# Optimization experiments

Measured on AMD Instinct MI355X. Metric: run time of the kernel, lower is better.

The kernel has to match this reference:

```python
import jax, jax.numpy as jnp
import numpy as np

H = 128
OUT = 3
N_C = 50000
N_F = 150000
E_C = 400000
N_MP = 2


def _layernorm(x, g, b, eps=1e-5):
    mu = jnp.mean(x, axis=-1, keepdims=True)
    xc = x - mu
    var = jnp.mean(xc * xc, axis=-1, keepdims=True)
    return xc * jax.lax.rsqrt(var + eps) * g + b


def _seg_mean(v, idx, n):
    s = jax.ops.segment_sum(v, idx, num_segments=n)
    c = jax.ops.segment_sum(jnp.ones((v.shape[0],), v.dtype), idx, num_segments=n)
    return s / jnp.maximum(c, 1.0)[:, None]


def _mp_pass(x, ea, ei, n_nodes, eW0, eb0, eW1, eb1, eg, ebt, nW0, nb0, nW1, nb1, ng, nbt):
    src, dst = ei[0], ei[1]
    for i in range(N_MP):
        # edge update: gather endpoints, concat, 2-layer MLP, residual + LN
        t = jnp.concatenate([x[src], x[dst], ea], axis=1)  # [E, 3H]
        t = jax.nn.elu(t @ eW0[i] + eb0[i])
        t = t @ eW1[i] + eb1[i]
        ea = _layernorm(ea + t, eg[i], ebt[i])
        # scatter-mean aggregate edges to target nodes (EdgeAggregator)
        agg = _seg_mean(ea, dst, n_nodes)  # [N, H]
        xt = jnp.concatenate([x, agg], axis=1)  # [N, 2H]
        xt = jax.nn.elu(xt @ nW0[i] + nb0[i])
        xt = xt @ nW1[i] + nb1[i]
        x = _layernorm(x + xt, ng[i], nbt[i])
    return x, ea


def setup_inputs() -> dict:
    key = jax.random.key(0)
    ks = jax.random.split(key, 40)

    def nrm(k, shape, fan):
        return jax.random.normal(k, shape, jnp.float32) * np.float32(1.0 / np.sqrt(fan))

    inp = {}
    inp["x"] = jax.random.normal(ks[0], (N_C, H), jnp.float32)
    inp["edge_attr"] = jax.random.normal(ks[1], (E_C, H), jnp.float32)
    inp["pos_c"] = jax.random.uniform(ks[2], (N_C, 2), jnp.float32)
    inp["pos_f"] = jax.random.uniform(ks[3], (N_F, 2), jnp.float32)
    inp["edge_index_c"] = jax.random.randint(ks[4], (2, E_C), 0, N_C)
    clusters = jax.random.randint(ks[5], (N_F,), 0, N_C)
    inp["clusters"] = clusters
    # one f2c edge per fine node: row0 = fine idx, row1 = its coarse cluster
    inp["edge_index_f2c"] = jnp.stack([jnp.arange(N_F), clusters])
    # edge_up_mps params (stacked over N_MP layers)
    inp["eW0"] = nrm(ks[6], (N_MP, 3 * H, H), 3 * H)
    inp["eb0"] = jnp.zeros((N_MP, H), jnp.float32)
    inp["eW1"] = nrm(ks[7], (N_MP, H, H), H)
    inp["eb1"] = jnp.zeros((N_MP, H), jnp.float32)
    inp["eg"] = jnp.ones((N_MP, H), jnp.float32)
    inp["ebt"] = jnp.zeros((N_MP, H), jnp.float32)
    # node_up_mps params
    inp["nW0"] = nrm(ks[8], (N_MP, 2 * H, H), 2 * H)
    inp["nb0"] = jnp.zeros((N_MP, H), jnp.float32)
    inp["nW1"] = nrm(ks[9], (N_MP, H, H), H)
    inp["nb1"] = jnp.zeros((N_MP, H), jnp.float32)
    inp["ng"] = jnp.ones((N_MP, H), jnp.float32)
    inp["nbt"] = jnp.zeros((N_MP, H), jnp.float32)
    # edge_decoder_c2f_mlp
    inp["dW0"] = nrm(ks[10], (2, H), 2)
    inp["db0"] = jnp.zeros((H,), jnp.float32)
    inp["dW1"] = nrm(ks[11], (H, H), H)
    inp["db1"] = jnp.zeros((H,), jnp.float32)
    # upsample_mlp + norm
    inp["uW0"] = nrm(ks[12], (2 * H, H), 2 * H)
    inp["ub0"] = jnp.zeros((H,), jnp.float32)
    inp["uW1"] = nrm(ks[13], (H, H), H)
    inp["ub1"] = jnp.zeros((H,), jnp.float32)
    inp["ug"] = jnp.ones((H,), jnp.float32)
    inp["ubt"] = jnp.zeros((H,), jnp.float32)
    # output embedding
    inp["oW"] = nrm(ks[14], (H, OUT), H)
    inp["ob"] = jnp.zeros((OUT,), jnp.float32)
    return inp


def reference(x, edge_attr, pos_c, pos_f, edge_index_c, clusters, edge_index_f2c,
              eW0, eb0, eW1, eb1, eg, ebt, nW0, nb0, nW1, nb1, ng, nbt,
              dW0, db0, dW1, db1, uW0, ub0, uW1, ub1, ug, ubt, oW, ob):
    # coarse-level message passing (m = 0)
    x, ea = _mp_pass(x, edge_attr, edge_index_c, N_C,
                     eW0, eb0, eW1, eb1, eg, ebt, nW0, nb0, nW1, nb1, ng, nbt)
    # upsample coarse -> fine (depth = 2, l_char[0] = 1.0)
    c2f = edge_index_f2c[::-1]  # row0 = coarse idx, row1 = fine idx
    eac = (pos_c[c2f[0]] - pos_f[c2f[1]]) / 1.0  # [N_F, 2]
    eac = jax.nn.elu(eac @ dW0 + db0)
    eac = jax.nn.elu(eac @ dW1 + db1)
    xg = x[clusters]  # [N_F, H]
    t = jnp.concatenate([eac, xg], axis=1)
    t = jax.nn.elu(t @ uW0 + ub0)
    t = jax.nn.elu(t @ uW1 + ub1)
    t = _layernorm(eac + t, ug, ubt)
    x = _seg_mean(t, c2f[1], N_F)  # aggregate c2f edges onto fine nodes
    # fine-level message passing (m stays 0 in the original code -> same weights, same coarse edges)
    x, ea = _mp_pass(x, ea, edge_index_c, N_F,
                     eW0, eb0, eW1, eb1, eg, ebt, nW0, nb0, nW1, nb1, ng, nbt)
    x = jax.nn.elu(x @ oW + ob)
    return (x, edge_index_c)
```

## Files before the change

### kernel.cpp

```cpp
#include <hip/hip_runtime.h>


#define HD   128
#define NC   50000
#define NF   150000
#define ECNT 400000
#define OUTD 3
#define SCB  512
#define NB_SCAN ((NF + SCB - 1) / SCB)

typedef unsigned short u16;
typedef unsigned int   u32;
typedef short bf16x8 __attribute__((ext_vector_type(8)));
typedef float f32x4  __attribute__((ext_vector_type(4)));

__device__ __forceinline__ float bf2f(u32 u){ return __uint_as_float(u << 16); }
__device__ __forceinline__ u32 cvtpk(float a, float b){
  u32 r; asm("v_cvt_pk_bf16_f32 %0, %1, %2" : "=v"(r) : "v"(a), "v"(b)); return r;
}
__device__ __forceinline__ u16 f2bf(float f){ return (u16)cvtpk(f, f); }
__device__ __forceinline__ u32 addpk(u32 a, u32 b){
  return cvtpk(bf2f(a & 0xffffu) + bf2f(b & 0xffffu),
               __uint_as_float(a & 0xffff0000u) + __uint_as_float(b & 0xffff0000u));
}
__device__ __forceinline__ float eluf(float x){ return x > 0.f ? x : __expf(x) - 1.f; }
__device__ __forceinline__ int SW(int row, int byte){ return row * 256 + (byte ^ ((row & 7) << 4)); }


__global__ void prep_all_kernel(const float* __restrict__ eW0, const float* __restrict__ eW1,
                                const float* __restrict__ nW0, const float* __restrict__ nW1,
                                const float* __restrict__ uW0, const float* __restrict__ uW1,
                                const float* __restrict__ dW1,
                                u16* c_eW0, u16* c_eW1, u16* c_nW0, u16* c_nW1,
                                u16* c_uW0, u16* c_uW1, u16* c_dW1)
{
  int b = blockIdx.x;
  const float* src; u16* dst; int kb;
  if      (b <  384){ src = eW0; dst = c_eW0; kb = b * 2; }
  else if (b <  512){ src = eW1; dst = c_eW1; kb = (b - 384) * 2; }
  else if (b <  768){ src = nW0; dst = c_nW0; kb = (b - 512) * 2; }
  else if (b <  896){ src = nW1; dst = c_nW1; kb = (b - 768) * 2; }
  else if (b < 1024){ src = uW0; dst = c_uW0; kb = (b - 896) * 2; }
  else if (b < 1088){ src = uW1; dst = c_uW1; kb = (b - 1024) * 2; }
  else              { src = dW1; dst = c_dW1; kb = (b - 1088) * 2; }
  int t = threadIdx.x;
  int k = kb + (t >> 7), j = t & 127;
  dst[(((k >> 3) * HD + j) << 3) + (k & 7)] = f2bf(src[k * HD + j]);
}

__global__ void f32_to_bf16_vec(const float* __restrict__ in, u16* __restrict__ out, int n8){
  int i = blockIdx.x * blockDim.x + threadIdx.x;
  if (i >= n8) return;
  float4 f0 = ((const float4*)in)[i * 2];
  float4 f1 = ((const float4*)in)[i * 2 + 1];
  ((uint4*)out)[i] = make_uint4(cvtpk(f0.x,f0.y), cvtpk(f0.z,f0.w), cvtpk(f1.x,f1.y), cvtpk(f1.z,f1.w));
}

__global__ void deg_kernel(const int* __restrict__ ei, int* __restrict__ deg){
  int e = blockIdx.x * blockDim.x + threadIdx.x;
  if (e < ECNT) atomicAdd(&deg[ei[ECNT + e]], 1);
}

__global__ void scanA_kernel(const int* __restrict__ deg, int* __restrict__ part){
  __shared__ int s[SCB];
  int t = threadIdx.x, i = blockIdx.x * SCB + t;
  s[t] = (i < NF) ? deg[i] : 0;
  __syncthreads();
  for (int off = SCB/2; off; off >>= 1){ if (t < off) s[t] += s[t + off]; __syncthreads(); }
  if (t == 0) part[blockIdx.x] = s[0];
}

__global__ void scanB_kernel(int* __restrict__ part){
  __shared__ int s[SCB];
  int t = threadIdx.x;
  int v = (t < NB_SCAN) ? part[t] : 0;
  s[t] = v; __syncthreads();
  for (int off = 1; off < SCB; off <<= 1){
    int x = (t >= off) ? s[t - off] : 0;
    __syncthreads(); s[t] += x; __syncthreads();
  }
  if (t < NB_SCAN) part[t] = s[t] - v;
}

__global__ void scanC_kernel(const int* __restrict__ deg, const int* __restrict__ part,
                             int* __restrict__ rowptr){
  __shared__ int s[SCB];
  int t = threadIdx.x, i = blockIdx.x * SCB + t;
  int v = (i < NF) ? deg[i] : 0;
  s[t] = v; __syncthreads();
  for (int off = 1; off < SCB; off <<= 1){
    int x = (t >= off) ? s[t - off] : 0;
    __syncthreads(); s[t] += x; __syncthreads();
  }
  int excl = part[blockIdx.x] + s[t] - v;
  if (i < NF) rowptr[i] = excl;
  if (i == NF - 1) rowptr[NF] = excl + v;
}

__global__ void build_perm_kernel(const int* __restrict__ ei, int* __restrict__ cursor,
                                  int* __restrict__ perm, int* __restrict__ esrc,
                                  int* __restrict__ edst){
  int e = blockIdx.x * blockDim.x + threadIdx.x;
  if (e >= ECNT) return;
  int sI = ei[e], d = ei[ECNT + e];
  int p = atomicAdd(&cursor[d], 1);
  perm[p] = e; esrc[p] = sI; edst[p] = d;
}

__global__ void permute_ea_kernel(const float* __restrict__ ea_in, const int* __restrict__ perm,
                                  u16* __restrict__ ea_s){
  int i = blockIdx.x * blockDim.x + threadIdx.x;
  if (i >= ECNT * 16) return;
  int p = i >> 4, c = i & 15;
  int e = perm[p];
  const float4* src = (const float4*)(ea_in + (size_t)e * HD + c * 8);
  float4 f0 = src[0], f1 = src[1];
  ((uint4*)ea_s)[(size_t)p * 16 + c] =
      make_uint4(cvtpk(f0.x,f0.y), cvtpk(f0.z,f0.w), cvtpk(f1.x,f1.y), cvtpk(f1.z,f1.w));
}

template<int NOUT>
__global__ __launch_bounds__(256, 4)
void lin_kernel(const u16* __restrict__ Wa, const u16* __restrict__ Wb, const u16* __restrict__ Wc,
                const u16* __restrict__ x, u16* __restrict__ oA, u16* __restrict__ oB,
                u16* __restrict__ oC, int nA, int nB, int nC, int n_rows)
{
  __shared__ __align__(16) char ldsA[32 * 256];
  const int tid = threadIdx.x, lane = tid & 63, wid = tid >> 6;
  const int ln = lane & 15, kq = lane >> 4, ncol = wid * 32;

  const int row0 = blockIdx.x << 5;
  #pragma unroll
  for (int c = 0; c < 2; ++c){
    int i = tid + c * 256, row = i >> 4, kk = i & 15, rg = row0 + row;
    if (rg < n_rows)
      *(uint4*)(ldsA + SW(row, kk * 16)) = *(const uint4*)(x + (((size_t)rg) << 7) + (kk << 3));
  }
  __syncthreads();
  bf16x8 af[4][2];
  #pragma unroll
  for (int k0 = 0; k0 < 4; ++k0){
    af[k0][0] = *(const bf16x8*)(ldsA + SW(ln,      k0 * 64 + (kq << 4)));
    af[k0][1] = *(const bf16x8*)(ldsA + SW(16 + ln, k0 * 64 + (kq << 4)));
  }

  const u16* Ws[3] = {Wa, Wb, Wc};
  u16*       Os[3] = {oA, oB, oC};
  const int  Ns[3] = {nA, nB, nC};
  const f32x4 zz = {0.f, 0.f, 0.f, 0.f};
  #pragma unroll
  for (int w = 0; w < NOUT; ++w){
    if (row0 < Ns[w]){
      const u16* wp = Ws[w];
      asm volatile("" : "+v"(wp));
      uint4 bfr[4][2];
      #pragma unroll
      for (int k0 = 0; k0 < 4; ++k0)
        #pragma unroll
        for (int nt = 0; nt < 2; ++nt)
          bfr[k0][nt] = *(const uint4*)(wp + (((size_t)((k0*4 + kq)*HD + ncol + nt*16 + ln)) << 3));
      f32x4 cc[2][2] = {{zz, zz}, {zz, zz}};
      #pragma unroll
      for (int k0 = 0; k0 < 4; ++k0){
        bf16x8 w0 = __builtin_bit_cast(bf16x8, bfr[k0][0]);
        bf16x8 w1 = __builtin_bit_cast(bf16x8, bfr[k0][1]);
        cc[0][0] = __builtin_amdgcn_mfma_f32_16x16x32_bf16(af[k0][0], w0, cc[0][0], 0, 0, 0);
        cc[0][1] = __builtin_amdgcn_mfma_f32_16x16x32_bf16(af[k0][0], w1, cc[0][1], 0, 0, 0);
        cc[1][0] = __builtin_amdgcn_mfma_f32_16x16x32_bf16(af[k0][1], w0, cc[1][0], 0, 0, 0);
        cc[1][1] = __builtin_amdgcn_mfma_f32_16x16x32_bf16(af[k0][1], w1, cc[1][1], 0, 0, 0);
      }
      u16* op = Os[w];
      #pragma unroll
      for (int mi = 0; mi < 2; ++mi)
        #pragma unroll
        for (int nt = 0; nt < 2; ++nt)
          #pragma unroll
          for (int r = 0; r < 4; ++r){
            int rg = row0 + mi * 16 + kq * 4 + r;
            if (rg < Ns[w]) op[(size_t)rg * HD + ncol + nt * 16 + ln] = f2bf(cc[mi][nt][r]);
          }
    }
  }
}

enum { M_EDGE = 0, M_NODE = 1, M_DEC12 = 2 };

template<int MODE>
__global__ __launch_bounds__(256, 4)
void mlp_kernel(const u16* __restrict__ W0c, const u16* __restrict__ W1c,
                const u16* __restrict__ W2c,
                const float* __restrict__ b0, const float* __restrict__ b1,
                const float* __restrict__ b2,
                const float* __restrict__ gw, const float* __restrict__ bw,
                const u16* __restrict__ tabA, const u16* __restrict__ addP,
                const u16* __restrict__ addQ, const u16* __restrict__ resid,
                const int* __restrict__ esrc, const int* __restrict__ edst,
                const int* __restrict__ rowptr, const u16* __restrict__ eatab,
                const int* __restrict__ clus,
                u16* __restrict__ outp, int n_rows,
                const float* __restrict__ dW0, const float* __restrict__ db0,
                const float* __restrict__ pos_c, const float* __restrict__ pos_f)
{
  constexpr bool RESLDS = (MODE == M_EDGE || MODE == M_DEC12);

  __shared__ __align__(16) char ldsA [32 * 256];
  __shared__ __align__(16) char ldsPQ[32 * 256];

  const int tid  = threadIdx.x;
  const int lane = tid & 63;
  const int wid  = tid >> 6;
  const int ln   = lane & 15, kq = lane >> 4;
  const int ncol = wid * 32;

  bf16x8 b1f[4][2];
  #pragma unroll
  for (int k0 = 0; k0 < 4; ++k0)
    #pragma unroll
    for (int nt = 0; nt < 2; ++nt)
      b1f[k0][nt] = *(const bf16x8*)(W0c + (((size_t)((k0*4 + kq)*HD + ncol + nt*16 + ln)) << 3));

  float b0v[2], b1v[2], b2v[2] = {0.f, 0.f};
  #pragma unroll
  for (int nt = 0; nt < 2; ++nt){ b0v[nt] = b0[ncol + nt*16 + ln]; b1v[nt] = b1[ncol + nt*16 + ln]; }
  if constexpr (MODE == M_DEC12){
    #pragma unroll
    for (int nt = 0; nt < 2; ++nt) b2v[nt] = b2[ncol + nt*16 + ln];
  }
  float gl0 = gw[lane], gl1 = gw[64 + lane], bt0 = bw[lane], bt1 = bw[64 + lane];

  const int row0 = blockIdx.x << 5;

  if constexpr (MODE == M_EDGE){
    #pragma unroll
    for (int c = 0; c < 2; ++c){
      int i = tid + c * 256, row = i >> 4, kk = i & 15, rg = row0 + row;
      *(uint4*)(ldsA + SW(row, kk * 16)) =
          *(const uint4*)(tabA + (((size_t)rg) << 7) + (kk << 3));
      int sI = esrc[rg], dI = edst[rg];
      uint4 p = *(const uint4*)(addP + (((size_t)sI) << 7) + (kk << 3));
      uint4 q = *(const uint4*)(addQ + (((size_t)dI) << 7) + (kk << 3));
      *(uint4*)(ldsPQ + SW(row, kk * 16)) =
          make_uint4(addpk(p.x,q.x), addpk(p.y,q.y), addpk(p.z,q.z), addpk(p.w,q.w));
    }
  } else if constexpr (MODE == M_NODE){
    #pragma unroll
    for (int c = 0; c < 2; ++c){
      int i = tid + c * 256, row = i >> 4, kk = i & 15, rg = row0 + row;
      if (rg < n_rows)
        *(uint4*)(ldsPQ + SW(row, kk * 16)) =
            *(const uint4*)(addP + (((size_t)rg) << 7) + (kk << 3));
    }
    for (int s = 0; s < 8; ++s){
      int nd = wid * 8 + s, rg = row0 + nd;
      if (rg < n_rows){
        int rp0 = rowptr[rg], rp1 = rowptr[rg + 1];
        float s0 = 0.f, s1 = 0.f, t0 = 0.f, t1 = 0.f;
        int i2 = rp0;
        for (; i2 + 3 < rp1; i2 += 4){
          u32 ua = *(const u32*)(eatab + (((size_t) i2     ) << 7) + (lane << 1));
          u32 ub = *(const u32*)(eatab + (((size_t)(i2 + 1)) << 7) + (lane << 1));
          u32 uc = *(const u32*)(eatab + (((size_t)(i2 + 2)) << 7) + (lane << 1));
          u32 ud = *(const u32*)(eatab + (((size_t)(i2 + 3)) << 7) + (lane << 1));
          s0 += bf2f(ua & 0xffffu) + bf2f(ub & 0xffffu);
          s1 += bf2f(ua >> 16)     + bf2f(ub >> 16);
          t0 += bf2f(uc & 0xffffu) + bf2f(ud & 0xffffu);
          t1 += bf2f(uc >> 16)     + bf2f(ud >> 16);
        }
        for (; i2 < rp1; ++i2){
          u32 ua = *(const u32*)(eatab + (((size_t)i2) << 7) + (lane << 1));
          s0 += bf2f(ua & 0xffffu); s1 += bf2f(ua >> 16);
        }
        s0 += t0; s1 += t1;
        int dg = rp1 - rp0;
        float rd = 1.f / (float)(dg > 0 ? dg : 1);
        *(u32*)(ldsA + SW(nd, lane << 2)) = cvtpk(s0 * rd, s1 * rd);
      }
    }
  } else {
    #pragma unroll
    for (int c = 0; c < 2; ++c){
      int i = tid + c * 256, row = i >> 4, c8 = i & 15, rg = row0 + row;
      if (rg < n_rows){
        int cl = clus[rg];
        *(uint4*)(ldsPQ + SW(row, c8 * 16)) =
            *(const uint4*)(addP + (((size_t)cl) << 7) + (c8 << 3));
        float d0 = pos_c[cl * 2]     - pos_f[rg * 2];
        float d1 = pos_c[cl * 2 + 1] - pos_f[rg * 2 + 1];
        u32 wq[4];
        #pragma unroll
        for (int q = 0; q < 4; ++q){
          int cc = c8 * 8 + q * 2;
          float va = eluf(fmaf(d0, dW0[cc],     fmaf(d1, dW0[HD + cc],     db0[cc])));
          float vb = eluf(fmaf(d0, dW0[cc + 1], fmaf(d1, dW0[HD + cc + 1], db0[cc + 1])));
          wq[q] = cvtpk(va, vb);
        }
        *(uint4*)(ldsA + SW(row, c8 * 16)) = make_uint4(wq[0], wq[1], wq[2], wq[3]);
      }
    }
  }
  __syncthreads();

  const f32x4 zz = {0.f, 0.f, 0.f, 0.f};
  f32x4 c1[2][2] = {{zz, zz}, {zz, zz}};
  #pragma unroll
  for (int k0 = 0; k0 < 4; ++k0){
    bf16x8 a0 = *(const bf16x8*)(ldsA + SW(ln,      k0 * 64 + (kq << 4)));
    bf16x8 a1 = *(const bf16x8*)(ldsA + SW(16 + ln, k0 * 64 + (kq << 4)));
    c1[0][0] = __builtin_amdgcn_mfma_f32_16x16x32_bf16(a0, b1f[k0][0], c1[0][0], 0, 0, 0);
    c1[0][1] = __builtin_amdgcn_mfma_f32_16x16x32_bf16(a0, b1f[k0][1], c1[0][1], 0, 0, 0);
    c1[1][0] = __builtin_amdgcn_mfma_f32_16x16x32_bf16(a1, b1f[k0][0], c1[1][0], 0, 0, 0);
    c1[1][1] = __builtin_amdgcn_mfma_f32_16x16x32_bf16(a1, b1f[k0][1], c1[1][1], 0, 0, 0);
  }

  if constexpr (MODE == M_DEC12){
    __syncthreads();
    #pragma unroll
    for (int mi = 0; mi < 2; ++mi)
      #pragma unroll
      for (int nt = 0; nt < 2; ++nt)
        #pragma unroll
        for (int r = 0; r < 4; ++r){
          int row = mi * 16 + kq * 4 + r, col = ncol + nt * 16 + ln;
          *(u16*)(ldsA + SW(row, col * 2)) = f2bf(eluf(c1[mi][nt][r] + b0v[nt]));
        }
    __syncthreads();

    {
      const u16* w1p = W1c;
      asm volatile("" : "+v"(w1p));
      uint4 b2r[4][2];
      #pragma unroll
      for (int k0 = 0; k0 < 4; ++k0)
        #pragma unroll
        for (int nt = 0; nt < 2; ++nt)
          b2r[k0][nt] = *(const uint4*)(w1p + (((size_t)((k0*4 + kq)*HD + ncol + nt*16 + ln)) << 3));
      f32x4 c2[2][2] = {{zz, zz}, {zz, zz}};
      #pragma unroll
      for (int k0 = 0; k0 < 4; ++k0){
        bf16x8 a0 = *(const bf16x8*)(ldsA + SW(ln,      k0 * 64 + (kq << 4)));
        bf16x8 a1 = *(const bf16x8*)(ldsA + SW(16 + ln, k0 * 64 + (kq << 4)));
        bf16x8 w0 = __builtin_bit_cast(bf16x8, b2r[k0][0]);
        bf16x8 w1 = __builtin_bit_cast(bf16x8, b2r[k0][1]);
        c2[0][0] = __builtin_amdgcn_mfma_f32_16x16x32_bf16(a0, w0, c2[0][0], 0, 0, 0);
        c2[0][1] = __builtin_amdgcn_mfma_f32_16x16x32_bf16(a0, w1, c2[0][1], 0, 0, 0);
        c2[1][0] = __builtin_amdgcn_mfma_f32_16x16x32_bf16(a1, w0, c2[1][0], 0, 0, 0);
        c2[1][1] = __builtin_amdgcn_mfma_f32_16x16x32_bf16(a1, w1, c2[1][1], 0, 0, 0);
      }
      #pragma unroll
      for (int mi = 0; mi < 2; ++mi)
        #pragma unroll
        for (int nt = 0; nt < 2; ++nt)
          #pragma unroll
          for (int r = 0; r < 4; ++r){
            int row = mi * 16 + kq * 4 + r, col = ncol + nt * 16 + ln;
            u16* pp = (u16*)(ldsPQ + SW(row, col * 2));
            float pq = bf2f(*pp);
            *pp = f2bf(eluf(c2[mi][nt][r] + pq + b1v[nt]));
          }
    }
    __syncthreads();

    {
      const u16* w2p = W2c;
      asm volatile("" : "+v"(w2p));
      uint4 b3r[4][2];
      #pragma unroll
      for (int k0 = 0; k0 < 4; ++k0)
        #pragma unroll
        for (int nt = 0; nt < 2; ++nt)
          b3r[k0][nt] = *(const uint4*)(w2p + (((size_t)((k0*4 + kq)*HD + ncol + nt*16 + ln)) << 3));
      f32x4 c3[2][2] = {{zz, zz}, {zz, zz}};
      #pragma unroll
      for (int k0 = 0; k0 < 4; ++k0){
        bf16x8 a0 = *(const bf16x8*)(ldsPQ + SW(ln,      k0 * 64 + (kq << 4)));
        bf16x8 a1 = *(const bf16x8*)(ldsPQ + SW(16 + ln, k0 * 64 + (kq << 4)));
        bf16x8 w0 = __builtin_bit_cast(bf16x8, b3r[k0][0]);
        bf16x8 w1 = __builtin_bit_cast(bf16x8, b3r[k0][1]);
        c3[0][0] = __builtin_amdgcn_mfma_f32_16x16x32_bf16(a0, w0, c3[0][0], 0, 0, 0);
        c3[0][1] = __builtin_amdgcn_mfma_f32_16x16x32_bf16(a0, w1, c3[0][1], 0, 0, 0);
        c3[1][0] = __builtin_amdgcn_mfma_f32_16x16x32_bf16(a1, w0, c3[1][0], 0, 0, 0);
        c3[1][1] = __builtin_amdgcn_mfma_f32_16x16x32_bf16(a1, w1, c3[1][1], 0, 0, 0);
      }
      __syncthreads();
      #pragma unroll
      for (int mi = 0; mi < 2; ++mi)
        #pragma unroll
        for (int nt = 0; nt < 2; ++nt)
          #pragma unroll
          for (int r = 0; r < 4; ++r){
            int row = mi * 16 + kq * 4 + r, col = ncol + nt * 16 + ln;
            *(u16*)(ldsPQ + SW(row, col * 2)) = f2bf(eluf(c3[mi][nt][r] + b2v[nt]));
          }
    }
    __syncthreads();
  } else {
    const u16* w1p = W1c;
    asm volatile("" : "+v"(w1p));
    uint4 b2r[4][2];
    #pragma unroll
    for (int k0 = 0; k0 < 4; ++k0)
      #pragma unroll
      for (int nt = 0; nt < 2; ++nt)
        b2r[k0][nt] = *(const uint4*)(w1p + (((size_t)((k0*4 + kq)*HD + ncol + nt*16 + ln)) << 3));

    #pragma unroll
    for (int mi = 0; mi < 2; ++mi)
      #pragma unroll
      for (int nt = 0; nt < 2; ++nt)
        #pragma unroll
        for (int r = 0; r < 4; ++r){
          int row = mi * 16 + kq * 4 + r, col = ncol + nt * 16 + ln;
          u16* pp = (u16*)(ldsPQ + SW(row, col * 2));
          float pq = bf2f(*pp);
          *pp = f2bf(eluf(c1[mi][nt][r] + pq + b0v[nt]));
        }
    __syncthreads();

    f32x4 c2[2][2] = {{zz, zz}, {zz, zz}};
    #pragma unroll
    for (int k0 = 0; k0 < 4; ++k0){
      bf16x8 a0 = *(const bf16x8*)(ldsPQ + SW(ln,      k0 * 64 + (kq << 4)));
      bf16x8 a1 = *(const bf16x8*)(ldsPQ + SW(16 + ln, k0 * 64 + (kq << 4)));
      bf16x8 w0 = __builtin_bit_cast(bf16x8, b2r[k0][0]);
      bf16x8 w1 = __builtin_bit_cast(bf16x8, b2r[k0][1]);
      c2[0][0] = __builtin_amdgcn_mfma_f32_16x16x32_bf16(a0, w0, c2[0][0], 0, 0, 0);
      c2[0][1] = __builtin_amdgcn_mfma_f32_16x16x32_bf16(a0, w1, c2[0][1], 0, 0, 0);
      c2[1][0] = __builtin_amdgcn_mfma_f32_16x16x32_bf16(a1, w0, c2[1][0], 0, 0, 0);
      c2[1][1] = __builtin_amdgcn_mfma_f32_16x16x32_bf16(a1, w1, c2[1][1], 0, 0, 0);
    }
    __syncthreads();

    #pragma unroll
    for (int mi = 0; mi < 2; ++mi)
      #pragma unroll
      for (int nt = 0; nt < 2; ++nt)
        #pragma unroll
        for (int r = 0; r < 4; ++r){
          int row = mi * 16 + kq * 4 + r, col = ncol + nt * 16 + ln;
          *(u16*)(ldsPQ + SW(row, col * 2)) = f2bf(c2[mi][nt][r] + b1v[nt]);
        }
    __syncthreads();
  }

  #pragma unroll
  for (int rr = 0; rr < 8; ++rr){
    int e = wid * 8 + rr, rg = row0 + e;
    float v0 = bf2f(*(const u16*)(ldsPQ + SW(e, lane * 2)));
    float v1 = bf2f(*(const u16*)(ldsPQ + SW(e, (64 + lane) * 2)));
    if constexpr (RESLDS){
      v0 += bf2f(*(const u16*)(ldsA + SW(e, lane * 2)));
      v1 += bf2f(*(const u16*)(ldsA + SW(e, (64 + lane) * 2)));
    } else if (rg < n_rows){
      v0 += bf2f(resid[(((size_t)rg) << 7) + lane]);
      v1 += bf2f(resid[(((size_t)rg) << 7) + 64 + lane]);
    }
    float s = v0 + v1, q = v0 * v0 + v1 * v1;
    #pragma unroll
    for (int o = 32; o; o >>= 1){ s += __shfl_xor(s, o); q += __shfl_xor(q, o); }
    float mu  = s * (1.f / 128.f);
    float var = q * (1.f / 128.f) - mu * mu;
    float rs  = rsqrtf(var + 1e-5f);
    float y0 = (v0 - mu) * rs * gl0 + bt0;
    float y1 = (v1 - mu) * rs * gl1 + bt1;
    if (rg < n_rows){
      outp[(((size_t)rg) << 7) + lane]      = f2bf(y0);
      outp[(((size_t)rg) << 7) + 64 + lane] = f2bf(y1);
    }
  }
}

__global__ void outhead_kernel(const u16* __restrict__ x, const float* __restrict__ oW,
                               const float* __restrict__ ob, float* __restrict__ out){
  int row  = (blockIdx.x * blockDim.x + threadIdx.x) >> 6;
  int lane = threadIdx.x & 63;
  if (row >= NF) return;
  float x0 = bf2f(x[((size_t)row << 7) + lane]);
  float x1 = bf2f(x[((size_t)row << 7) + 64 + lane]);
  float s0 = x0 * oW[lane * 3 + 0] + x1 * oW[(64 + lane) * 3 + 0];
  float s1 = x0 * oW[lane * 3 + 1] + x1 * oW[(64 + lane) * 3 + 1];
  float s2 = x0 * oW[lane * 3 + 2] + x1 * oW[(64 + lane) * 3 + 2];
  #pragma unroll
  for (int o = 32; o; o >>= 1){
    s0 += __shfl_xor(s0, o); s1 += __shfl_xor(s1, o); s2 += __shfl_xor(s2, o);
  }
  if (lane == 0){
    out[row * 3 + 0] = eluf(s0 + ob[0]);
    out[row * 3 + 1] = eluf(s1 + ob[1]);
    out[row * 3 + 2] = eluf(s2 + ob[2]);
  }
}

__global__ void idxcopy_kernel(const int* __restrict__ ei, float* __restrict__ out){
  int i = blockIdx.x * blockDim.x + threadIdx.x;
  if (i < 2 * ECNT) out[i] = (float)ei[i];
}

extern "C" void kernel_launch(void* const* d_in, const int* in_sizes, int n_in,
                              void* d_out, int out_size, void* d_ws, size_t ws_size,
                              hipStream_t stream)
{
  const float* x_in  = (const float*)d_in[0];
  const float* ea_in = (const float*)d_in[1];
  const float* pos_c = (const float*)d_in[2];
  const float* pos_f = (const float*)d_in[3];
  const int*   ei    = (const int*)d_in[4];
  const int*   clus  = (const int*)d_in[5];
  const float* eW0 = (const float*)d_in[7];
  const float* eb0 = (const float*)d_in[8];
  const float* eW1 = (const float*)d_in[9];
  const float* eb1 = (const float*)d_in[10];
  const float* eg  = (const float*)d_in[11];
  const float* ebt = (const float*)d_in[12];
  const float* nW0 = (const float*)d_in[13];
  const float* nb0 = (const float*)d_in[14];
  const float* nW1 = (const float*)d_in[15];
  const float* nb1 = (const float*)d_in[16];
  const float* ng  = (const float*)d_in[17];
  const float* nbt = (const float*)d_in[18];
  const float* dW0 = (const float*)d_in[19];
  const float* db0 = (const float*)d_in[20];
  const float* dW1 = (const float*)d_in[21];
  const float* db1 = (const float*)d_in[22];
  const float* uW0 = (const float*)d_in[23];
  const float* ub0 = (const float*)d_in[24];
  const float* uW1 = (const float*)d_in[25];
  const float* ub1 = (const float*)d_in[26];
  const float* ug  = (const float*)d_in[27];
  const float* ubt = (const float*)d_in[28];
  const float* oW  = (const float*)d_in[29];
  const float* ob  = (const float*)d_in[30];

  char* w = (char*)d_ws;
  auto alloc = [&](size_t bytes) -> char* {
    char* p = w; w += (bytes + 255) & ~(size_t)255; return p;
  };
  u16*   ea_s   = (u16*)alloc((size_t)ECNT * HD * 2);
  u16*   xa     = (u16*)alloc((size_t)NC * HD * 2);
  u16*   xb     = (u16*)alloc((size_t)NF * HD * 2);
  u16*   P      = (u16*)alloc((size_t)NF * HD * 2);
  u16*   Q      = (u16*)alloc((size_t)NF * HD * 2);
  u16*   T      = (u16*)alloc((size_t)NF * HD * 2);
  u16*   XU     = (u16*)alloc((size_t)NC * HD * 2);
  int*   deg    = (int*)alloc((size_t)NF * 4);
  int*   rowptr = (int*)alloc((size_t)(NF + 1) * 4);
  int*   cursor = (int*)alloc((size_t)NF * 4);
  int*   perm   = (int*)alloc((size_t)ECNT * 4);
  int*   esrc   = (int*)alloc((size_t)ECNT * 4);
  int*   edst   = (int*)alloc((size_t)ECNT * 4);
  int*   part   = (int*)alloc((size_t)SCB * 4);
  u16*   c_eW0  = (u16*)alloc((size_t)2 * 384 * HD * 2);
  u16*   c_eW1  = (u16*)alloc((size_t)2 * HD * HD * 2);
  u16*   c_nW0  = (u16*)alloc((size_t)2 * 256 * HD * 2);
  u16*   c_nW1  = (u16*)alloc((size_t)2 * HD * HD * 2);
  u16*   c_uW0  = (u16*)alloc((size_t)256 * HD * 2);
  u16*   c_uW1  = (u16*)alloc((size_t)HD * HD * 2);
  u16*   c_dW1  = (u16*)alloc((size_t)HD * HD * 2);

  prep_all_kernel<<<1152, 256, 0, stream>>>(eW0, eW1, nW0, nW1, uW0, uW1, dW1,
                                            c_eW0, c_eW1, c_nW0, c_nW1, c_uW0, c_uW1, c_dW1);
  f32_to_bf16_vec<<<(NC * HD / 8 + 255) / 256, 256, 0, stream>>>(x_in, xa, NC * HD / 8);

  hipMemsetAsync(deg, 0, (size_t)NF * 4, stream);
  deg_kernel<<<(ECNT + 255) / 256, 256, 0, stream>>>(ei, deg);
  scanA_kernel<<<NB_SCAN, SCB, 0, stream>>>(deg, part);
  scanB_kernel<<<1, SCB, 0, stream>>>(part);
  scanC_kernel<<<NB_SCAN, SCB, 0, stream>>>(deg, part, rowptr);
  hipMemcpyAsync(cursor, rowptr, (size_t)NF * 4, hipMemcpyDeviceToDevice, stream);
  build_perm_kernel<<<(ECNT + 255) / 256, 256, 0, stream>>>(ei, cursor, perm, esrc, edst);
  permute_ea_kernel<<<(ECNT * 16 + 255) / 256, 256, 0, stream>>>(ea_in, perm, ea_s);

  auto grd = [](int rows){ return (rows + 31) / 32; };
  const int KS = 16 * HD * 8;

  auto mp_iter = [&](u16* x, int n, int i){
    int npq = n < NC ? n : NC;
    lin_kernel<3><<<grd(n), 256, 0, stream>>>(
      c_eW0 + (size_t)i*384*HD, c_eW0 + (size_t)i*384*HD + KS, c_nW0 + (size_t)i*256*HD,
      x, P, Q, T, npq, npq, n, n);
    mlp_kernel<M_EDGE><<<grd(ECNT), 256, 0, stream>>>(
      c_eW0 + (size_t)i*384*HD + 2*KS, c_eW1 + (size_t)i*HD*HD, nullptr,
      eb0 + i*HD, eb1 + i*HD, nullptr, eg + i*HD, ebt + i*HD,
      ea_s, P, Q, nullptr, esrc, edst, nullptr, nullptr, nullptr,
      ea_s, ECNT, nullptr, nullptr, nullptr, nullptr);
    mlp_kernel<M_NODE><<<grd(n), 256, 0, stream>>>(
      c_nW0 + (size_t)i*256*HD + KS, c_nW1 + (size_t)i*HD*HD, nullptr,
      nb0 + i*HD, nb1 + i*HD, nullptr, ng + i*HD, nbt + i*HD,
      nullptr, T, nullptr, x, nullptr, nullptr, rowptr, ea_s, nullptr,
      x, n, nullptr, nullptr, nullptr, nullptr);
  };

  mp_iter(xa, NC, 0);
  mp_iter(xa, NC, 1);

  lin_kernel<1><<<grd(NC), 256, 0, stream>>>(
    c_uW0 + KS, nullptr, nullptr, xa, XU, nullptr, nullptr, NC, 0, 0, NC);
  mlp_kernel<M_DEC12><<<grd(NF), 256, 0, stream>>>(
    c_dW1, c_uW0, c_uW1,
    db1, ub0, ub1, ug, ubt,
    nullptr, XU, nullptr, nullptr,
    nullptr, nullptr, nullptr, nullptr, clus,
    xb, NF, dW0, db0, pos_c, pos_f);

  mp_iter(xb, NF, 0);
  mp_iter(xb, NF, 1);

  float* out = (float*)d_out;
  outhead_kernel<<<(NF + 3) / 4, 256, 0, stream>>>(xb, oW, ob, out);
  idxcopy_kernel<<<(2 * ECNT + 255) / 256, 256, 0, stream>>>(ei, out + (size_t)NF * OUTD);
}
```

Before: 983.0 us.

## Fuse node-side x@W0 projection into node MLP kernel and skip aggregation for edgeless rows

```diff
diff --git a/kernel.cpp b/kernel.cpp
--- a/kernel.cpp
+++ b/kernel.cpp
@@ -121,9 +121,9 @@
 
 template<int NOUT>
 __global__ __launch_bounds__(256, 4)
-void lin_kernel(const u16* __restrict__ Wa, const u16* __restrict__ Wb, const u16* __restrict__ Wc,
+void lin_kernel(const u16* __restrict__ Wa, const u16* __restrict__ Wb,
                 const u16* __restrict__ x, u16* __restrict__ oA, u16* __restrict__ oB,
-                u16* __restrict__ oC, int nA, int nB, int nC, int n_rows)
+                int n_rows)
 {
   __shared__ __align__(16) char ldsA[32 * 256];
   const int tid = threadIdx.x, lane = tid & 63, wid = tid >> 6;
@@ -144,42 +144,39 @@
     af[k0][1] = *(const bf16x8*)(ldsA + SW(16 + ln, k0 * 64 + (kq << 4)));
   }
 
-  const u16* Ws[3] = {Wa, Wb, Wc};
-  u16*       Os[3] = {oA, oB, oC};
-  const int  Ns[3] = {nA, nB, nC};
+  const u16* Ws[2] = {Wa, Wb};
+  u16*       Os[2] = {oA, oB};
   const f32x4 zz = {0.f, 0.f, 0.f, 0.f};
   #pragma unroll
   for (int w = 0; w < NOUT; ++w){
-    if (row0 < Ns[w]){
-      const u16* wp = Ws[w];
-      asm volatile("" : "+v"(wp));
-      uint4 bfr[4][2];
-      #pragma unroll
-      for (int k0 = 0; k0 < 4; ++k0)
-        #pragma unroll
-        for (int nt = 0; nt < 2; ++nt)
-          bfr[k0][nt] = *(const uint4*)(wp + (((size_t)((k0*4 + kq)*HD + ncol + nt*16 + ln)) << 3));
-      f32x4 cc[2][2] = {{zz, zz}, {zz, zz}};
-      #pragma unroll
-      for (int k0 = 0; k0 < 4; ++k0){
-        bf16x8 w0 = __builtin_bit_cast(bf16x8, bfr[k0][0]);
-        bf16x8 w1 = __builtin_bit_cast(bf16x8, bfr[k0][1]);
-        cc[0][0] = __builtin_amdgcn_mfma_f32_16x16x32_bf16(af[k0][0], w0, cc[0][0], 0, 0, 0);
-        cc[0][1] = __builtin_amdgcn_mfma_f32_16x16x32_bf16(af[k0][0], w1, cc[0][1], 0, 0, 0);
-        cc[1][0] = __builtin_amdgcn_mfma_f32_16x16x32_bf16(af[k0][1], w0, cc[1][0], 0, 0, 0);
-        cc[1][1] = __builtin_amdgcn_mfma_f32_16x16x32_bf16(af[k0][1], w1, cc[1][1], 0, 0, 0);
-      }
-      u16* op = Os[w];
-      #pragma unroll
-      for (int mi = 0; mi < 2; ++mi)
-        #pragma unroll
-        for (int nt = 0; nt < 2; ++nt)
-          #pragma unroll
-          for (int r = 0; r < 4; ++r){
-            int rg = row0 + mi * 16 + kq * 4 + r;
-            if (rg < Ns[w]) op[(size_t)rg * HD + ncol + nt * 16 + ln] = f2bf(cc[mi][nt][r]);
-          }
-    }
+    const u16* wp = Ws[w];
+    asm volatile("" : "+v"(wp));
+    uint4 bfr[4][2];
+    #pragma unroll
+    for (int k0 = 0; k0 < 4; ++k0)
+      #pragma unroll
+      for (int nt = 0; nt < 2; ++nt)
+        bfr[k0][nt] = *(const uint4*)(wp + (((size_t)((k0*4 + kq)*HD + ncol + nt*16 + ln)) << 3));
+    f32x4 cc[2][2] = {{zz, zz}, {zz, zz}};
+    #pragma unroll
+    for (int k0 = 0; k0 < 4; ++k0){
+      bf16x8 w0 = __builtin_bit_cast(bf16x8, bfr[k0][0]);
+      bf16x8 w1 = __builtin_bit_cast(bf16x8, bfr[k0][1]);
+      cc[0][0] = __builtin_amdgcn_mfma_f32_16x16x32_bf16(af[k0][0], w0, cc[0][0], 0, 0, 0);
+      cc[0][1] = __builtin_amdgcn_mfma_f32_16x16x32_bf16(af[k0][0], w1, cc[0][1], 0, 0, 0);
+      cc[1][0] = __builtin_amdgcn_mfma_f32_16x16x32_bf16(af[k0][1], w0, cc[1][0], 0, 0, 0);
+      cc[1][1] = __builtin_amdgcn_mfma_f32_16x16x32_bf16(af[k0][1], w1, cc[1][1], 0, 0, 0);
+    }
+    u16* op = Os[w];
+    #pragma unroll
+    for (int mi = 0; mi < 2; ++mi)
+      #pragma unroll
+      for (int nt = 0; nt < 2; ++nt)
+        #pragma unroll
+        for (int r = 0; r < 4; ++r){
+          int rg = row0 + mi * 16 + kq * 4 + r;
+          if (rg < n_rows) op[(size_t)rg * HD + ncol + nt * 16 + ln] = f2bf(cc[mi][nt][r]);
+        }
   }
 }
 
@@ -247,34 +244,8 @@
     for (int c = 0; c < 2; ++c){
       int i = tid + c * 256, row = i >> 4, kk = i & 15, rg = row0 + row;
       if (rg < n_rows)
-        *(uint4*)(ldsPQ + SW(row, kk * 16)) =
-            *(const uint4*)(addP + (((size_t)rg) << 7) + (kk << 3));
-    }
-    for (int s = 0; s < 8; ++s){
-      int nd = wid * 8 + s, rg = row0 + nd;
-      if (rg < n_rows){
-        int rp0 = rowptr[rg], rp1 = rowptr[rg + 1];
-        float s0 = 0.f, s1 = 0.f, t0 = 0.f, t1 = 0.f;
-        int i2 = rp0;
-        for (; i2 + 3 < rp1; i2 += 4){
-          u32 ua = *(const u32*)(eatab + (((size_t) i2     ) << 7) + (lane << 1));
-          u32 ub = *(const u32*)(eatab + (((size_t)(i2 + 1)) << 7) + (lane << 1));
-          u32 uc = *(const u32*)(eatab + (((size_t)(i2 + 2)) << 7) + (lane << 1));
-          u32 ud = *(const u32*)(eatab + (((size_t)(i2 + 3)) << 7) + (lane << 1));
-          s0 += bf2f(ua & 0xffffu) + bf2f(ub & 0xffffu);
-          s1 += bf2f(ua >> 16)     + bf2f(ub >> 16);
-          t0 += bf2f(uc & 0xffffu) + bf2f(ud & 0xffffu);
-          t1 += bf2f(uc >> 16)     + bf2f(ud >> 16);
-        }
-        for (; i2 < rp1; ++i2){
-          u32 ua = *(const u32*)(eatab + (((size_t)i2) << 7) + (lane << 1));
-          s0 += bf2f(ua & 0xffffu); s1 += bf2f(ua >> 16);
-        }
-        s0 += t0; s1 += t1;
-        int dg = rp1 - rp0;
-        float rd = 1.f / (float)(dg > 0 ? dg : 1);
-        *(u32*)(ldsA + SW(nd, lane << 2)) = cvtpk(s0 * rd, s1 * rd);
-      }
+        *(uint4*)(ldsA + SW(row, kk * 16)) =
+            *(const uint4*)(tabA + (((size_t)rg) << 7) + (kk << 3));
     }
   } else {
     #pragma unroll
@@ -390,6 +361,103 @@
           for (int r = 0; r < 4; ++r){
             int row = mi * 16 + kq * 4 + r, col = ncol + nt * 16 + ln;
             *(u16*)(ldsPQ + SW(row, col * 2)) = f2bf(eluf(c3[mi][nt][r] + b2v[nt]));
+          }
+    }
+    __syncthreads();
+  } else if constexpr (MODE == M_NODE){
+    __syncthreads();
+    const bool act = (row0 < NC);
+    if (act){
+      for (int s = 0; s < 8; ++s){
+        int nd = wid * 8 + s, rg = row0 + nd;
+        if (rg < n_rows){
+          int rp0 = rowptr[rg], rp1 = rowptr[rg + 1];
+          float s0 = 0.f, s1 = 0.f, t0 = 0.f, t1 = 0.f;
+          int i2 = rp0;
+          for (; i2 + 3 < rp1; i2 += 4){
+            u32 ua = *(const u32*)(eatab + (((size_t) i2     ) << 7) + (lane << 1));
+            u32 ub = *(const u32*)(eatab + (((size_t)(i2 + 1)) << 7) + (lane << 1));
+            u32 uc = *(const u32*)(eatab + (((size_t)(i2 + 2)) << 7) + (lane << 1));
+            u32 ud = *(const u32*)(eatab + (((size_t)(i2 + 3)) << 7) + (lane << 1));
+            s0 += bf2f(ua & 0xffffu) + bf2f(ub & 0xffffu);
+            s1 += bf2f(ua >> 16)     + bf2f(ub >> 16);
+            t0 += bf2f(uc & 0xffffu) + bf2f(ud & 0xffffu);
+            t1 += bf2f(uc >> 16)     + bf2f(ud >> 16);
+          }
+          for (; i2 < rp1; ++i2){
+            u32 ua = *(const u32*)(eatab + (((size_t)i2) << 7) + (lane << 1));
+            s0 += bf2f(ua & 0xffffu); s1 += bf2f(ua >> 16);
+          }
+          s0 += t0; s1 += t1;
+          int dg = rp1 - rp0;
+          float rd = 1.f / (float)(dg > 0 ? dg : 1);
+          *(u32*)(ldsA + SW(nd, lane << 2)) = cvtpk(s0 * rd, s1 * rd);
+        }
+      }
+    }
+    __syncthreads();
+    if (act){
+      const u16* wbp = W1c;
+      asm volatile("" : "+v"(wbp));
+      uint4 bbr[4][2];
+      #pragma unroll
+      for (int k0 = 0; k0 < 4; ++k0)
+        #pragma unroll
+        for (int nt = 0; nt < 2; ++nt)
+          bbr[k0][nt] = *(const uint4*)(wbp + (((size_t)((k0*4 + kq)*HD + ncol + nt*16 + ln)) << 3));
+      #pragma unroll
+      for (int k0 = 0; k0 < 4; ++k0){
+        bf16x8 a0 = *(const bf16x8*)(ldsA + SW(ln,      k0 * 64 + (kq << 4)));
+        bf16x8 a1 = *(const bf16x8*)(ldsA + SW(16 + ln, k0 * 64 + (kq << 4)));
+        bf16x8 w0 = __builtin_bit_cast(bf16x8, bbr[k0][0]);
+        bf16x8 w1 = __builtin_bit_cast(bf16x8, bbr[k0][1]);
+        c1[0][0] = __builtin_amdgcn_mfma_f32_16x16x32_bf16(a0, w0, c1[0][0], 0, 0, 0);
+        c1[0][1] = __builtin_amdgcn_mfma_f32_16x16x32_bf16(a0, w1, c1[0][1], 0, 0, 0);
+        c1[1][0] = __builtin_amdgcn_mfma_f32_16x16x32_bf16(a1, w0, c1[1][0], 0, 0, 0);
+        c1[1][1] = __builtin_amdgcn_mfma_f32_16x16x32_bf16(a1, w1, c1[1][1], 0, 0, 0);
+      }
+    }
+    #pragma unroll
+    for (int mi = 0; mi < 2; ++mi)
+      #pragma unroll
+      for (int nt = 0; nt < 2; ++nt)
+        #pragma unroll
+        for (int r = 0; r < 4; ++r){
+          int row = mi * 16 + kq * 4 + r, col = ncol + nt * 16 + ln;
+          *(u16*)(ldsPQ + SW(row, col * 2)) = f2bf(eluf(c1[mi][nt][r] + b0v[nt]));
+        }
+    __syncthreads();
+
+    {
+      const u16* w2p = W2c;
+      asm volatile("" : "+v"(w2p));
+      uint4 b3r[4][2];
+      #pragma unroll
+      for (int k0 = 0; k0 < 4; ++k0)
+        #pragma unroll
+        for (int nt = 0; nt < 2; ++nt)
+          b3r[k0][nt] = *(const uint4*)(w2p + (((size_t)((k0*4 + kq)*HD + ncol + nt*16 + ln)) << 3));
+      f32x4 c2[2][2] = {{zz, zz}, {zz, zz}};
+      #pragma unroll
+      for (int k0 = 0; k0 < 4; ++k0){
+        bf16x8 a0 = *(const bf16x8*)(ldsPQ + SW(ln,      k0 * 64 + (kq << 4)));
+        bf16x8 a1 = *(const bf16x8*)(ldsPQ + SW(16 + ln, k0 * 64 + (kq << 4)));
+        bf16x8 w0 = __builtin_bit_cast(bf16x8, b3r[k0][0]);
+        bf16x8 w1 = __builtin_bit_cast(bf16x8, b3r[k0][1]);
+        c2[0][0] = __builtin_amdgcn_mfma_f32_16x16x32_bf16(a0, w0, c2[0][0], 0, 0, 0);
+        c2[0][1] = __builtin_amdgcn_mfma_f32_16x16x32_bf16(a0, w1, c2[0][1], 0, 0, 0);
+        c2[1][0] = __builtin_amdgcn_mfma_f32_16x16x32_bf16(a1, w0, c2[1][0], 0, 0, 0);
+        c2[1][1] = __builtin_amdgcn_mfma_f32_16x16x32_bf16(a1, w1, c2[1][1], 0, 0, 0);
+      }
+      __syncthreads();
+      #pragma unroll
+      for (int mi = 0; mi < 2; ++mi)
+        #pragma unroll
+        for (int nt = 0; nt < 2; ++nt)
+          #pragma unroll
+          for (int r = 0; r < 4; ++r){
+            int row = mi * 16 + kq * 4 + r, col = ncol + nt * 16 + ln;
+            *(u16*)(ldsPQ + SW(row, col * 2)) = f2bf(c2[mi][nt][r] + b1v[nt]);
           }
     }
     __syncthreads();
@@ -537,9 +605,8 @@
   u16*   ea_s   = (u16*)alloc((size_t)ECNT * HD * 2);
   u16*   xa     = (u16*)alloc((size_t)NC * HD * 2);
   u16*   xb     = (u16*)alloc((size_t)NF * HD * 2);
-  u16*   P      = (u16*)alloc((size_t)NF * HD * 2);
-  u16*   Q      = (u16*)alloc((size_t)NF * HD * 2);
-  u16*   T      = (u16*)alloc((size_t)NF * HD * 2);
+  u16*   P      = (u16*)alloc((size_t)NC * HD * 2);
+  u16*   Q      = (u16*)alloc((size_t)NC * HD * 2);
   u16*   XU     = (u16*)alloc((size_t)NC * HD * 2);
   int*   deg    = (int*)alloc((size_t)NF * 4);
   int*   rowptr = (int*)alloc((size_t)(NF + 1) * 4);
@@ -574,18 +641,17 @@
 
   auto mp_iter = [&](u16* x, int n, int i){
     int npq = n < NC ? n : NC;
-    lin_kernel<3><<<grd(n), 256, 0, stream>>>(
-      c_eW0 + (size_t)i*384*HD, c_eW0 + (size_t)i*384*HD + KS, c_nW0 + (size_t)i*256*HD,
-      x, P, Q, T, npq, npq, n, n);
+    lin_kernel<2><<<grd(npq), 256, 0, stream>>>(
+      c_eW0 + (size_t)i*384*HD, c_eW0 + (size_t)i*384*HD + KS, x, P, Q, npq);
     mlp_kernel<M_EDGE><<<grd(ECNT), 256, 0, stream>>>(
       c_eW0 + (size_t)i*384*HD + 2*KS, c_eW1 + (size_t)i*HD*HD, nullptr,
       eb0 + i*HD, eb1 + i*HD, nullptr, eg + i*HD, ebt + i*HD,
       ea_s, P, Q, nullptr, esrc, edst, nullptr, nullptr, nullptr,
       ea_s, ECNT, nullptr, nullptr, nullptr, nullptr);
     mlp_kernel<M_NODE><<<grd(n), 256, 0, stream>>>(
-      c_nW0 + (size_t)i*256*HD + KS, c_nW1 + (size_t)i*HD*HD, nullptr,
+      c_nW0 + (size_t)i*256*HD, c_nW0 + (size_t)i*256*HD + KS, c_nW1 + (size_t)i*HD*HD,
       nb0 + i*HD, nb1 + i*HD, nullptr, ng + i*HD, nbt + i*HD,
-      nullptr, T, nullptr, x, nullptr, nullptr, rowptr, ea_s, nullptr,
+      x, nullptr, nullptr, x, nullptr, nullptr, rowptr, ea_s, nullptr,
       x, n, nullptr, nullptr, nullptr, nullptr);
   };
 
@@ -593,7 +659,7 @@
   mp_iter(xa, NC, 1);
 
   lin_kernel<1><<<grd(NC), 256, 0, stream>>>(
-    c_uW0 + KS, nullptr, nullptr, xa, XU, nullptr, nullptr, NC, 0, 0, NC);
+    c_uW0 + KS, nullptr, xa, XU, nullptr, NC);
   mlp_kernel<M_DEC12><<<grd(NF), 256, 0, stream>>>(
     c_dW1, c_uW0, c_uW1,
     db1, ub0, ub1, ug, ubt,
```

Measured after the change: 888.3 us. 1.11x faster.
